# Optimization experiments

Measured on AMD Instinct MI355X. Metric: run time of the kernel, lower is better.

Reference implementation:

```python
import jax, jax.numpy as jnp
import numpy as np

B, S, HID, NH, MAX_TOKENS = 2, 2048, 2048, 16, 2048
HD = HID // NH

def rotate_half(x):
    x1, x2 = x[..., :x.shape[-1] // 2], x[..., x.shape[-1] // 2:]
    return jnp.concatenate((-x2, x1), axis=-1)

def rope_tables():
    inv_freq = 1.0 / (10000.0 ** (jnp.arange(0, HD, 2, dtype=jnp.float32) / HD))
    t = jnp.arange(MAX_TOKENS, dtype=jnp.float32)
    freqs = jnp.outer(t, inv_freq)                       # [T, HD/2]
    emb = jnp.concatenate((freqs, freqs), axis=-1)       # [T, HD]
    return jnp.cos(emb), jnp.sin(emb)

def setup_inputs() -> dict:
    key = jax.random.key(0)
    ks = jax.random.split(key, 5)
    hidden_states = jax.random.normal(ks[0], (B, S, HID), dtype=jnp.float32)
    # additive causal mask [B, 1, S, S]: 0 on/below diag, large negative above
    neg = jnp.finfo(jnp.float32).min
    causal = jnp.where(jnp.tril(jnp.ones((S, S), dtype=bool)), 0.0, neg)
    attention_mask = jnp.broadcast_to(causal[None, None], (B, 1, S, S)).astype(jnp.float32)
    position_ids = jnp.broadcast_to(jnp.arange(S, dtype=jnp.int32), (B, S))
    scale = 1.0 / np.sqrt(HID)
    Wq = jax.random.normal(ks[1], (HID, HID), dtype=jnp.float32) * scale
    Wk = jax.random.normal(ks[2], (HID, HID), dtype=jnp.float32) * scale
    Wv = jax.random.normal(ks[3], (HID, HID), dtype=jnp.float32) * scale
    Wo = jax.random.normal(ks[4], (HID, HID), dtype=jnp.float32) * scale
    return {"hidden_states": hidden_states, "attention_mask": attention_mask,
            "position_ids": position_ids, "Wq": Wq, "Wk": Wk, "Wv": Wv, "Wo": Wo}

def reference(hidden_states, attention_mask, position_ids, Wq, Wk, Wv, Wo):
    b, s, _ = hidden_states.shape
    def proj(W):  # torch Linear: x @ W.T -> [b, H, s, hd]
        return (hidden_states @ W.T).reshape(b, s, NH, HD).transpose(0, 2, 1, 3)
    q, k, v = proj(Wq), proj(Wk), proj(Wv)
    cos_t, sin_t = rope_tables()
    cos = cos_t[position_ids][:, None]   # [b, 1, s, hd]
    sin = sin_t[position_ids][:, None]
    q = q * cos + rotate_half(q) * sin
    k = k * cos + rotate_half(k) * sin
    scores = jnp.einsum('bhqd,bhkd->bhqk', q, k) / np.sqrt(HD)
    scores = jnp.maximum(scores + attention_mask, jnp.finfo(scores.dtype).min)
    attn = jax.nn.softmax(scores.astype(jnp.float32), axis=-1).astype(q.dtype)
    out = jnp.einsum('bhqk,bhkd->bhqd', attn, v)
    out = out.transpose(0, 2, 1, 3).reshape(b, s, HID)
    return out @ Wo.T
```

## Files before the change

### kernel.cpp

```cpp
#include <hip/hip_runtime.h>

#define B_   2
#define S_   2048
#define HID_ 2048
#define NH_  16
#define HD_  128

typedef float  f32x4  __attribute__((ext_vector_type(4)));
typedef __bf16 bf16x8 __attribute__((ext_vector_type(8)));

__device__ __forceinline__ unsigned short f2bf(float f) {
  union { float fv; unsigned u; } v; v.fv = f;
  unsigned r = v.u + 0x7FFFu + ((v.u >> 16) & 1u);
  return (unsigned short)(r >> 16);
}
__device__ __forceinline__ float bf2f(unsigned short h) {
  union { unsigned u; float fv; } v; v.u = ((unsigned)h) << 16;
  return v.fv;
}

__device__ __forceinline__ void gload16(const void* g, void* lds) {
  __builtin_amdgcn_global_load_lds(
      (const __attribute__((address_space(1))) void*)g,
      (__attribute__((address_space(3))) void*)lds, 16, 0, 0);
}

#define H4_ (B_ * S_ * HID_ / 4)
#define W4_ (HID_ * HID_ / 4)
__global__ void cast_all(const float* __restrict__ h,  const float* __restrict__ wq,
                         const float* __restrict__ wk, const float* __restrict__ wv,
                         const float* __restrict__ wo,
                         unsigned short* __restrict__ xb,  unsigned short* __restrict__ wqb,
                         unsigned short* __restrict__ wkb, unsigned short* __restrict__ wvb,
                         unsigned short* __restrict__ wob) {
  const int total = H4_ + 4 * W4_;
  int i = blockIdx.x * blockDim.x + threadIdx.x;
  int stride = gridDim.x * blockDim.x;
  for (; i < total; i += stride) {
    const float* src; unsigned short* dst; int j;
    if (i < H4_) { src = h; dst = xb; j = i; }
    else {
      int k = i - H4_, wsel = k >> 20;
      j = k & (W4_ - 1);
      src = (wsel == 0) ? wq : (wsel == 1) ? wk : (wsel == 2) ? wv : wo;
      dst = (wsel == 0) ? wqb : (wsel == 1) ? wkb : (wsel == 2) ? wvb : wob;
    }
    float4 v = ((const float4*)src)[j];
    ushort4 o;
    o.x = f2bf(v.x); o.y = f2bf(v.y); o.z = f2bf(v.z); o.w = f2bf(v.w);
    ((ushort4*)dst)[j] = o;
  }
}

template <int EPI>
__global__ __launch_bounds__(256, 2)
void gemm_bt(const unsigned short* __restrict__ A,
             const unsigned short* __restrict__ Bw,
             void* __restrict__ Cout, int M, int N, int K) {
  __shared__ __align__(16) unsigned short As[128 * 32];
  __shared__ __align__(16) unsigned short Bs[128 * 32];
  const int tid = threadIdx.x, lane = tid & 63, w = tid >> 6;
  const int n0 = blockIdx.x * 128, m0 = blockIdx.y * 128;
  const int wm = (w & 1) * 64, wn = (w >> 1) * 64;
  const int rowq = lane & 15;
  const int koff = (lane >> 4) * 8;
  const int lr0 = (lane >> 4) * 4;

  f32x4 acc[4][4];
  for (int i = 0; i < 4; ++i)
    for (int j = 0; j < 4; ++j)
      for (int r = 0; r < 4; ++r) acc[i][j][r] = 0.f;

  for (int k0 = 0; k0 < K; k0 += 32) {
    __syncthreads();
    for (int c = 0; c < 2; ++c) {
      int chunk = (w * 2 + c) * 64 + lane;
      int row = chunk >> 2, cc = chunk & 3;
      gload16(A + (size_t)(m0 + row) * K + k0 + cc * 8, As + (w * 2 + c) * 512);
      gload16(Bw + (size_t)(n0 + row) * K + k0 + cc * 8, Bs + (w * 2 + c) * 512);
    }
    __syncthreads();
    bf16x8 af[4], bfv[4];
    for (int i = 0; i < 4; ++i) {
      af[i]  = *(const bf16x8*)&As[(wm + i * 16 + rowq) * 32 + koff];
      bfv[i] = *(const bf16x8*)&Bs[(wn + i * 16 + rowq) * 32 + koff];
    }
    for (int mi = 0; mi < 4; ++mi)
      for (int ni = 0; ni < 4; ++ni)
        acc[mi][ni] = __builtin_amdgcn_mfma_f32_16x16x32_bf16(af[mi], bfv[ni], acc[mi][ni], 0, 0, 0);
  }

  for (int mi = 0; mi < 4; ++mi)
    for (int ni = 0; ni < 4; ++ni)
      for (int r = 0; r < 4; ++r) {
        int r_ = m0 + wm + mi * 16 + lr0 + r;
        int c_ = n0 + wn + ni * 16 + rowq;
        float v = acc[mi][ni][r];
        if (EPI == 0) {
          ((float*)Cout)[(size_t)r_ * N + c_] = v;
        } else if (EPI == 1) {
          ((unsigned short*)Cout)[(size_t)r_ * N + c_] = f2bf(v);
        } else {
          int b = r_ >> 11, s = r_ & 2047, h = c_ >> 7, d = c_ & 127;
          ((unsigned short*)Cout)[(((size_t)(b * NH_ + h) * S_ + s) * HD_) + d] = f2bf(v);
        }
      }
}

__global__ void rope_kernel(unsigned short* __restrict__ Qb,
                            unsigned short* __restrict__ Kb,
                            const int* __restrict__ pos_ids) {
  const int bhs = blockIdx.x;
  const int d = threadIdx.x;
  const int s = bhs & (S_ - 1);
  const int b = bhs >> 15;
  const int p = pos_ids[b * S_ + s];
  const float f = expf(-(float)d * (9.210340371976184f / 64.f));
  float sn, cs;
  sincosf((float)p * f, &sn, &cs);
  size_t base = (size_t)bhs * HD_;
  {
    float x1 = bf2f(Qb[base + d]), x2 = bf2f(Qb[base + d + 64]);
    Qb[base + d]      = f2bf(x1 * cs - x2 * sn);
    Qb[base + d + 64] = f2bf(x2 * cs + x1 * sn);
  }
  {
    float x1 = bf2f(Kb[base + d]), x2 = bf2f(Kb[base + d + 64]);
    Kb[base + d]      = f2bf(x1 * cs - x2 * sn);
    Kb[base + d + 64] = f2bf(x2 * cs + x1 * sn);
  }
}

__global__ __launch_bounds__(256)
void transpose_v(const unsigned short* __restrict__ Vin,
                 unsigned short* __restrict__ Vt) {
  __shared__ unsigned short t[64 * 66];
  const int s0 = blockIdx.x * 64, d0 = blockIdx.y * 64, bh = blockIdx.z;
  const int b = bh >> 4, h = bh & 15;
  for (int it = 0; it < 16; ++it) {
    int lin = it * 256 + threadIdx.x;
    int sl = lin >> 6, dl = lin & 63;
    t[sl * 66 + dl] = Vin[(size_t)(b * S_ + s0 + sl) * HID_ + h * HD_ + d0 + dl];
  }
  __syncthreads();
  for (int it = 0; it < 16; ++it) {
    int lin = it * 256 + threadIdx.x;
    int dl = lin >> 6, sl = lin & 63;
    Vt[((size_t)bh * HD_ + d0 + dl) * S_ + s0 + sl] = t[sl * 66 + dl];
  }
}

#define KS_LD 136
#define VS_LD 72
#define PS_LD 72
__global__ __launch_bounds__(256, 2)
void attn_fused(const unsigned short* __restrict__ Qb,
                const unsigned short* __restrict__ Kb,
                const unsigned short* __restrict__ Vt,
                unsigned short* __restrict__ Ob) {
  __shared__ __align__(16) unsigned short Ks[64 * KS_LD];
  __shared__ __align__(16) unsigned short Vts[128 * VS_LD];
  __shared__ __align__(16) unsigned short Ps[4 * 16 * PS_LD];

  const int tid = threadIdx.x, lane = tid & 63, w = tid >> 6;
  const int bh = blockIdx.x;
  const int qt = (gridDim.y - 1) - blockIdx.y;
  const int q0 = qt * 64;
  const int b = bh >> 4, h = bh & 15;
  const int rowq = lane & 15;
  const int koff = (lane >> 4) * 8;
  const int lr0 = (lane >> 4) * 4;
  const size_t qkbase = (size_t)bh * (S_ * HD_);
  const size_t vbase  = (size_t)bh * (HD_ * S_);

  bf16x8 qf0, qf1, qf2, qf3;
  {
    const unsigned short* qrow = Qb + qkbase + (size_t)(q0 + w * 16 + rowq) * HD_;
    qf0 = *(const bf16x8*)(qrow + 0 * 32 + koff);
    qf1 = *(const bf16x8*)(qrow + 1 * 32 + koff);
    qf2 = *(const bf16x8*)(qrow + 2 * 32 + koff);
    qf3 = *(const bf16x8*)(qrow + 3 * 32 + koff);
  }

  const int krow = tid >> 4, kcol = (tid & 15) * 8;
  const int vrow = tid >> 3, vcol = (tid & 7) * 8;
  const unsigned short* kptr = Kb + qkbase + (size_t)krow * HD_ + kcol;
  const unsigned short* vptr = Vt + vbase + (size_t)vrow * S_ + vcol;

  f32x4 oacc[8];
  for (int i = 0; i < 8; ++i)
    for (int r = 0; r < 4; ++r) oacc[i][r] = 0.f;
  float m_r[4] = {-3e38f, -3e38f, -3e38f, -3e38f};
  float l_r[4] = {0.f, 0.f, 0.f, 0.f};

  const int nkt = qt + 1;

  float4 k0, k1, k2, k3, v0, v1, v2, v3;
  k0 = *(const float4*)(kptr + 0 * 16 * HD_);
  k1 = *(const float4*)(kptr + 1 * 16 * HD_);
  k2 = *(const float4*)(kptr + 2 * 16 * HD_);
  k3 = *(const float4*)(kptr + 3 * 16 * HD_);
  v0 = *(const float4*)(vptr + 0 * 32 * S_);
  v1 = *(const float4*)(vptr + 1 * 32 * S_);
  v2 = *(const float4*)(vptr + 2 * 32 * S_);
  v3 = *(const float4*)(vptr + 3 * 32 * S_);

  for (int kt = 0; kt < nkt; ++kt) {
    __syncthreads();
    *(float4*)&Ks[(krow + 0 * 16) * KS_LD + kcol] = k0;
    *(float4*)&Ks[(krow + 1 * 16) * KS_LD + kcol] = k1;
    *(float4*)&Ks[(krow + 2 * 16) * KS_LD + kcol] = k2;
    *(float4*)&Ks[(krow + 3 * 16) * KS_LD + kcol] = k3;
    *(float4*)&Vts[(vrow + 0 * 32) * VS_LD + vcol] = v0;
    *(float4*)&Vts[(vrow + 1 * 32) * VS_LD + vcol] = v1;
    *(float4*)&Vts[(vrow + 2 * 32) * VS_LD + vcol] = v2;
    *(float4*)&Vts[(vrow + 3 * 32) * VS_LD + vcol] = v3;
    if (kt + 1 < nkt) {
      const unsigned short* kp = kptr + (size_t)(kt + 1) * 64 * HD_;
      k0 = *(const float4*)(kp + 0 * 16 * HD_);
      k1 = *(const float4*)(kp + 1 * 16 * HD_);
      k2 = *(const float4*)(kp + 2 * 16 * HD_);
      k3 = *(const float4*)(kp + 3 * 16 * HD_);
    }
    __syncthreads();

    f32x4 sacc[4];
    for (int n = 0; n < 4; ++n)
      for (int r = 0; r < 4; ++r) sacc[n][r] = 0.f;
#pragma unroll
    for (int n = 0; n < 4; ++n) {
      const unsigned short* krow_p = &Ks[(n * 16 + rowq) * KS_LD + koff];
      sacc[n] = __builtin_amdgcn_mfma_f32_16x16x32_bf16(qf0, *(const bf16x8*)(krow_p + 0 * 32), sacc[n], 0, 0, 0);
      sacc[n] = __builtin_amdgcn_mfma_f32_16x16x32_bf16(qf1, *(const bf16x8*)(krow_p + 1 * 32), sacc[n], 0, 0, 0);
      sacc[n] = __builtin_amdgcn_mfma_f32_16x16x32_bf16(qf2, *(const bf16x8*)(krow_p + 2 * 32), sacc[n], 0, 0, 0);
      sacc[n] = __builtin_amdgcn_mfma_f32_16x16x32_bf16(qf3, *(const bf16x8*)(krow_p + 3 * 32), sacc[n], 0, 0, 0);
    }

    const float scale = 0.08838834764831845f;
    float tmax[4] = {-3e38f, -3e38f, -3e38f, -3e38f};
    if (kt == qt) {
      for (int n = 0; n < 4; ++n) {
        int col = n * 16 + rowq;
        for (int r = 0; r < 4; ++r) {
          int row = w * 16 + lr0 + r;
          float x = sacc[n][r] * scale;
          x = (col <= row) ? x : -1e30f;
          sacc[n][r] = x;
          tmax[r] = fmaxf(tmax[r], x);
        }
      }
    } else {
      for (int n = 0; n < 4; ++n)
        for (int r = 0; r < 4; ++r) {
          float x = sacc[n][r] * scale;
          sacc[n][r] = x;
          tmax[r] = fmaxf(tmax[r], x);
        }
    }
    for (int off = 1; off < 16; off <<= 1)
      for (int r = 0; r < 4; ++r) tmax[r] = fmaxf(tmax[r], __shfl_xor(tmax[r], off));
    float alpha[4];
    for (int r = 0; r < 4; ++r) {
      float mn = fmaxf(m_r[r], tmax[r]);
      alpha[r] = __expf(m_r[r] - mn);
      m_r[r] = mn;
    }
    float rs[4] = {0.f, 0.f, 0.f, 0.f};
    for (int n = 0; n < 4; ++n)
      for (int r = 0; r < 4; ++r) {
        float p = __expf(sacc[n][r] - m_r[r]);
        sacc[n][r] = p;
        rs[r] += p;
      }
    for (int off = 1; off < 16; off <<= 1)
      for (int r = 0; r < 4; ++r) rs[r] += __shfl_xor(rs[r], off);
    for (int r = 0; r < 4; ++r) l_r[r] = l_r[r] * alpha[r] + rs[r];
    for (int nd = 0; nd < 8; ++nd)
      for (int r = 0; r < 4; ++r) oacc[nd][r] *= alpha[r];

    if (kt + 1 < nkt) {
      const unsigned short* vp = vptr + (size_t)(kt + 1) * 64;
      v0 = *(const float4*)(vp + 0 * 32 * S_);
      v1 = *(const float4*)(vp + 1 * 32 * S_);
      v2 = *(const float4*)(vp + 2 * 32 * S_);
      v3 = *(const float4*)(vp + 3 * 32 * S_);
    }

    unsigned short* pw = &Ps[w * 16 * PS_LD];
    for (int n = 0; n < 4; ++n)
      for (int r = 0; r < 4; ++r)
        pw[(lr0 + r) * PS_LD + n * 16 + rowq] = f2bf(sacc[n][r]);

#pragma unroll
    for (int t2 = 0; t2 < 2; ++t2) {
      bf16x8 pa = *(const bf16x8*)&pw[rowq * PS_LD + t2 * 32 + koff];
      for (int nd = 0; nd < 8; ++nd) {
        bf16x8 vb = *(const bf16x8*)&Vts[(nd * 16 + rowq) * VS_LD + t2 * 32 + koff];
        oacc[nd] = __builtin_amdgcn_mfma_f32_16x16x32_bf16(pa, vb, oacc[nd], 0, 0, 0);
      }
    }
  }

  float linv[4];
  for (int r = 0; r < 4; ++r) linv[r] = __builtin_amdgcn_rcpf(l_r[r]);
  for (int nd = 0; nd < 8; ++nd) {
    int col = h * HD_ + nd * 16 + rowq;
    for (int r = 0; r < 4; ++r) {
      int row = q0 + w * 16 + lr0 + r;
      Ob[(size_t)(b * S_ + row) * HID_ + col] = f2bf(oacc[nd][r] * linv[r]);
    }
  }
}

extern "C" void kernel_launch(void* const* d_in, const int* in_sizes, int n_in,
                              void* d_out, int out_size, void* d_ws, size_t ws_size,
                              hipStream_t stream) {
  (void)in_sizes; (void)n_in; (void)out_size; (void)ws_size;
  const float* hidden = (const float*)d_in[0];
  const int* pos = (const int*)d_in[2];
  const float* Wq = (const float*)d_in[3];
  const float* Wk = (const float*)d_in[4];
  const float* Wv = (const float*)d_in[5];
  const float* Wo = (const float*)d_in[6];
  float* out = (float*)d_out;

  char* ws = (char*)d_ws;
  unsigned short* Xb   = (unsigned short*)(ws);
  unsigned short* Wqb  = (unsigned short*)(ws + 16777216);
  unsigned short* Wkb  = (unsigned short*)(ws + 25165824);
  unsigned short* Wvb  = (unsigned short*)(ws + 33554432);
  unsigned short* Wob  = (unsigned short*)(ws + 41943040);
  unsigned short* Qb   = (unsigned short*)(ws + 50331648);
  unsigned short* Kb   = (unsigned short*)(ws + 67108864);
  unsigned short* Vtmp = (unsigned short*)(ws + 83886080);
  unsigned short* Vtb  = (unsigned short*)(ws + 100663296);
  unsigned short* Ob   = Xb;

  cast_all<<<2048, 256, 0, stream>>>(hidden, Wq, Wk, Wv, Wo, Xb, Wqb, Wkb, Wvb, Wob);

  dim3 gg(HID_ / 128, (B_ * S_) / 128);
  gemm_bt<2><<<gg, 256, 0, stream>>>(Xb, Wqb, Qb, B_ * S_, HID_, HID_);
  gemm_bt<2><<<gg, 256, 0, stream>>>(Xb, Wkb, Kb, B_ * S_, HID_, HID_);
  gemm_bt<1><<<gg, 256, 0, stream>>>(Xb, Wvb, Vtmp, B_ * S_, HID_, HID_);

  rope_kernel<<<B_ * NH_ * S_, 64, 0, stream>>>(Qb, Kb, pos);

  dim3 tg(S_ / 64, HD_ / 64, B_ * NH_);
  transpose_v<<<tg, 256, 0, stream>>>(Vtmp, Vtb);

  dim3 ag(B_ * NH_, S_ / 64);
  attn_fused<<<ag, 256, 0, stream>>>(Qb, Kb, Vtb, Ob);

  gemm_bt<0><<<gg, 256, 0, stream>>>(Ob, Wob, out, B_ * S_, HID_, HID_);
}
```

Before: 458.2 us.

## Fuse QKV projections into one GEMM, tabulate RoPE, fold softmax scale into Q

The three Q/K/V projection GEMMs become a single launch over a three-times-wider N dimension. This relies on the bf16 Wq/Wk/Wv copies sitting contiguously in the workspace, and the epilogue routes each column range to the Q, K or V layout. RoPE now reads a precomputed cos/sin table, built per call in reused workspace, instead of calling sincos for every element. The attention scale times log2(e) is folded into Q during RoPE, so the softmax drops its per-score multiply and uses exp2. The aim is fewer launches, a better-filled grid for the projections, and less ALU work in RoPE and softmax, at the cost of an extra small table kernel and one more bf16 rounding of the pre-scaled Q.

New measurement: 422.0 us. -7.9%, faster.

```diff
diff --git a/kernel.cpp b/kernel.cpp
--- a/kernel.cpp
+++ b/kernel.cpp
@@ -5,6 +5,7 @@
 #define HID_ 2048
 #define NH_  16
 #define HD_  128
+#define MAXTOK_ 2048
 
 typedef float  f32x4  __attribute__((ext_vector_type(4)));
 typedef __bf16 bf16x8 __attribute__((ext_vector_type(8)));
@@ -52,11 +53,14 @@
   }
 }
 
-template <int EPI>
+
 __global__ __launch_bounds__(256, 2)
-void gemm_bt(const unsigned short* __restrict__ A,
-             const unsigned short* __restrict__ Bw,
-             void* __restrict__ Cout, int M, int N, int K) {
+void gemm_qkv(const unsigned short* __restrict__ A,
+              const unsigned short* __restrict__ Bw,
+              unsigned short* __restrict__ Qb,
+              unsigned short* __restrict__ Kb,
+              unsigned short* __restrict__ Vtmp) {
+  const int K = HID_;
   __shared__ __align__(16) unsigned short As[128 * 32];
   __shared__ __align__(16) unsigned short Bs[128 * 32];
   const int tid = threadIdx.x, lane = tid & 63, w = tid >> 6;
@@ -96,38 +100,95 @@
         int r_ = m0 + wm + mi * 16 + lr0 + r;
         int c_ = n0 + wn + ni * 16 + rowq;
         float v = acc[mi][ni][r];
-        if (EPI == 0) {
-          ((float*)Cout)[(size_t)r_ * N + c_] = v;
-        } else if (EPI == 1) {
-          ((unsigned short*)Cout)[(size_t)r_ * N + c_] = f2bf(v);
+        int b = r_ >> 11, s = r_ & 2047;
+        int proj = c_ >> 11, cin = c_ & 2047;
+        if (proj == 2) {
+          Vtmp[(size_t)(b * S_ + s) * HID_ + cin] = f2bf(v);
         } else {
-          int b = r_ >> 11, s = r_ & 2047, h = c_ >> 7, d = c_ & 127;
-          ((unsigned short*)Cout)[(((size_t)(b * NH_ + h) * S_ + s) * HD_) + d] = f2bf(v);
+          int hh = cin >> 7, d = cin & 127;
+          unsigned short* dst = (proj == 0) ? Qb : Kb;
+          dst[(((size_t)(b * NH_ + hh) * S_ + s) * HD_) + d] = f2bf(v);
         }
       }
 }
 
-__global__ void rope_kernel(unsigned short* __restrict__ Qb,
-                            unsigned short* __restrict__ Kb,
-                            const int* __restrict__ pos_ids) {
-  const int bhs = blockIdx.x;
-  const int d = threadIdx.x;
-  const int s = bhs & (S_ - 1);
-  const int b = bhs >> 15;
-  const int p = pos_ids[b * S_ + s];
-  const float f = expf(-(float)d * (9.210340371976184f / 64.f));
+__global__ __launch_bounds__(256, 2)
+void gemm_out(const unsigned short* __restrict__ A,
+              const unsigned short* __restrict__ Bw,
+              float* __restrict__ Cout) {
+  const int N = HID_, K = HID_;
+  __shared__ __align__(16) unsigned short As[128 * 32];
+  __shared__ __align__(16) unsigned short Bs[128 * 32];
+  const int tid = threadIdx.x, lane = tid & 63, w = tid >> 6;
+  const int n0 = blockIdx.x * 128, m0 = blockIdx.y * 128;
+  const int wm = (w & 1) * 64, wn = (w >> 1) * 64;
+  const int rowq = lane & 15;
+  const int koff = (lane >> 4) * 8;
+  const int lr0 = (lane >> 4) * 4;
+
+  f32x4 acc[4][4];
+  for (int i = 0; i < 4; ++i)
+    for (int j = 0; j < 4; ++j)
+      for (int r = 0; r < 4; ++r) acc[i][j][r] = 0.f;
+
+  for (int k0 = 0; k0 < K; k0 += 32) {
+    __syncthreads();
+    for (int c = 0; c < 2; ++c) {
+      int chunk = (w * 2 + c) * 64 + lane;
+      int row = chunk >> 2, cc = chunk & 3;
+      gload16(A + (size_t)(m0 + row) * K + k0 + cc * 8, As + (w * 2 + c) * 512);
+      gload16(Bw + (size_t)(n0 + row) * K + k0 + cc * 8, Bs + (w * 2 + c) * 512);
+    }
+    __syncthreads();
+    bf16x8 af[4], bfv[4];
+    for (int i = 0; i < 4; ++i) {
+      af[i]  = *(const bf16x8*)&As[(wm + i * 16 + rowq) * 32 + koff];
+      bfv[i] = *(const bf16x8*)&Bs[(wn + i * 16 + rowq) * 32 + koff];
+    }
+    for (int mi = 0; mi < 4; ++mi)
+      for (int ni = 0; ni < 4; ++ni)
+        acc[mi][ni] = __builtin_amdgcn_mfma_f32_16x16x32_bf16(af[mi], bfv[ni], acc[mi][ni], 0, 0, 0);
+  }
+
+  for (int mi = 0; mi < 4; ++mi)
+    for (int ni = 0; ni < 4; ++ni)
+      for (int r = 0; r < 4; ++r) {
+        int r_ = m0 + wm + mi * 16 + lr0 + r;
+        int c_ = n0 + wn + ni * 16 + rowq;
+        Cout[(size_t)r_ * N + c_] = acc[mi][ni][r];
+      }
+}
+
+__global__ void rope_table(float2* __restrict__ tbl) {
+  int i = blockIdx.x * blockDim.x + threadIdx.x;
+  if (i >= MAXTOK_ * 64) return;
+  int p = i >> 6, d = i & 63;
+  float f = __expf(-(float)d * (9.210340371976184f / 64.f));
   float sn, cs;
-  sincosf((float)p * f, &sn, &cs);
+  __sincosf((float)p * f, &sn, &cs);
+  tbl[i] = make_float2(cs, sn);
+}
+
+#define QSCALE_ 0.12751744f
+__global__ __launch_bounds__(256)
+void rope_apply(unsigned short* __restrict__ Qb, unsigned short* __restrict__ Kb,
+                const int* __restrict__ pos_ids, const float2* __restrict__ tbl) {
+  int i = blockIdx.x * blockDim.x + threadIdx.x;
+  int d = i & 63, bhs = i >> 6;
+  int s = bhs & (S_ - 1);
+  int b = bhs >> 15;
+  int p = pos_ids[b * S_ + s];
+  float2 cssn = tbl[p * 64 + d];
   size_t base = (size_t)bhs * HD_;
   {
     float x1 = bf2f(Qb[base + d]), x2 = bf2f(Qb[base + d + 64]);
-    Qb[base + d]      = f2bf(x1 * cs - x2 * sn);
-    Qb[base + d + 64] = f2bf(x2 * cs + x1 * sn);
+    Qb[base + d]      = f2bf((x1 * cssn.x - x2 * cssn.y) * QSCALE_);
+    Qb[base + d + 64] = f2bf((x2 * cssn.x + x1 * cssn.y) * QSCALE_);
   }
   {
     float x1 = bf2f(Kb[base + d]), x2 = bf2f(Kb[base + d + 64]);
-    Kb[base + d]      = f2bf(x1 * cs - x2 * sn);
-    Kb[base + d + 64] = f2bf(x2 * cs + x1 * sn);
+    Kb[base + d]      = f2bf(x1 * cssn.x - x2 * cssn.y);
+    Kb[base + d + 64] = f2bf(x2 * cssn.x + x1 * cssn.y);
   }
 }
 
@@ -236,39 +297,34 @@
       sacc[n] = __builtin_amdgcn_mfma_f32_16x16x32_bf16(qf3, *(const bf16x8*)(krow_p + 3 * 32), sacc[n], 0, 0, 0);
     }
 
-    const float scale = 0.08838834764831845f;
     float tmax[4] = {-3e38f, -3e38f, -3e38f, -3e38f};
     if (kt == qt) {
       for (int n = 0; n < 4; ++n) {
         int col = n * 16 + rowq;
         for (int r = 0; r < 4; ++r) {
           int row = w * 16 + lr0 + r;
-          float x = sacc[n][r] * scale;
-          x = (col <= row) ? x : -1e30f;
+          float x = (col <= row) ? sacc[n][r] : -1e30f;
           sacc[n][r] = x;
           tmax[r] = fmaxf(tmax[r], x);
         }
       }
     } else {
       for (int n = 0; n < 4; ++n)
-        for (int r = 0; r < 4; ++r) {
-          float x = sacc[n][r] * scale;
-          sacc[n][r] = x;
-          tmax[r] = fmaxf(tmax[r], x);
-        }
+        for (int r = 0; r < 4; ++r)
+          tmax[r] = fmaxf(tmax[r], sacc[n][r]);
     }
     for (int off = 1; off < 16; off <<= 1)
       for (int r = 0; r < 4; ++r) tmax[r] = fmaxf(tmax[r], __shfl_xor(tmax[r], off));
     float alpha[4];
     for (int r = 0; r < 4; ++r) {
       float mn = fmaxf(m_r[r], tmax[r]);
-      alpha[r] = __expf(m_r[r] - mn);
+      alpha[r] = __builtin_amdgcn_exp2f(m_r[r] - mn);
       m_r[r] = mn;
     }
     float rs[4] = {0.f, 0.f, 0.f, 0.f};
     for (int n = 0; n < 4; ++n)
       for (int r = 0; r < 4; ++r) {
-        float p = __expf(sacc[n][r] - m_r[r]);
+        float p = __builtin_amdgcn_exp2f(sacc[n][r] - m_r[r]);
         sacc[n][r] = p;
         rs[r] += p;
       }
@@ -335,15 +391,15 @@
   unsigned short* Vtmp = (unsigned short*)(ws + 83886080);
   unsigned short* Vtb  = (unsigned short*)(ws + 100663296);
   unsigned short* Ob   = Xb;
+  float2* tbl          = (float2*)ws;
 
   cast_all<<<2048, 256, 0, stream>>>(hidden, Wq, Wk, Wv, Wo, Xb, Wqb, Wkb, Wvb, Wob);
 
-  dim3 gg(HID_ / 128, (B_ * S_) / 128);
-  gemm_bt<2><<<gg, 256, 0, stream>>>(Xb, Wqb, Qb, B_ * S_, HID_, HID_);
-  gemm_bt<2><<<gg, 256, 0, stream>>>(Xb, Wkb, Kb, B_ * S_, HID_, HID_);
-  gemm_bt<1><<<gg, 256, 0, stream>>>(Xb, Wvb, Vtmp, B_ * S_, HID_, HID_);
-
-  rope_kernel<<<B_ * NH_ * S_, 64, 0, stream>>>(Qb, Kb, pos);
+  dim3 gq(3 * HID_ / 128, (B_ * S_) / 128);
+  gemm_qkv<<<gq, 256, 0, stream>>>(Xb, Wqb, Qb, Kb, Vtmp);
+
+  rope_table<<<(MAXTOK_ * 64) / 256, 256, 0, stream>>>(tbl);
+  rope_apply<<<(B_ * NH_ * S_ * 64) / 256, 256, 0, stream>>>(Qb, Kb, pos, tbl);
 
   dim3 tg(S_ / 64, HD_ / 64, B_ * NH_);
   transpose_v<<<tg, 256, 0, stream>>>(Vtmp, Vtb);
@@ -351,5 +407,6 @@
   dim3 ag(B_ * NH_, S_ / 64);
   attn_fused<<<ag, 256, 0, stream>>>(Qb, Kb, Vtb, Ob);
 
-  gemm_bt<0><<<gg, 256, 0, stream>>>(Ob, Wob, out, B_ * S_, HID_, HID_);
-}
+  dim3 go(HID_ / 128, (B_ * S_) / 128);
+  gemm_out<<<go, 256, 0, stream>>>(Ob, Wob, out);
+}
```
